# Performance work log

Hardware: AMD Instinct MI355X
Metric: run time of the kernel (lower is better)

Reference implementation:

```python
import jax, jax.numpy as jnp
import numpy as np
from math import sqrt

D_MODEL = 1024
B, T = 4, 4096


def setup_inputs() -> dict:
    key = jax.random.key(0)
    kx, kqk, kvo = jax.random.split(key, 3)
    x = jax.random.normal(kx, (B, T, D_MODEL), dtype=jnp.float32)
    # xavier_uniform for square [D, D]: limit = sqrt(6 / (D + D))
    limit = sqrt(6.0 / (2 * D_MODEL))
    QK = jax.random.uniform(kqk, (D_MODEL, D_MODEL), minval=-limit, maxval=limit, dtype=jnp.float32)
    VO = jax.random.uniform(kvo, (D_MODEL, D_MODEL), minval=-limit, maxval=limit, dtype=jnp.float32)
    return {"x": x, "QK": QK, "VO": VO}


def reference(x, QK, VO):
    d_model = QK.shape[0]
    # scores[b,t,u] = x[b,t,:] @ QK @ x[b,u,:]  -- precompute xQK once
    xQK = jnp.einsum('btd,de->bte', x, QK)                 # [B,T,D]
    scores = jnp.einsum('bte,bue->btu', xQK, x) / sqrt(d_model)  # [B,T,T]
    attn = jax.nn.softmax(scores, axis=2)
    # out[b,t,e] = attn @ x @ VO
    av = jnp.einsum('btu,bud->btd', attn, x)               # [B,T,D]
    return jnp.einsum('btd,de->bte', av, VO)
```

## Files before the change

kernel.cpp:

```cpp
#include <hip/hip_runtime.h>
#include <hip/hip_bf16.h>


#define BB 4
#define TT 4096
#define DD 1024

typedef __attribute__((ext_vector_type(8))) short bf16x8;
typedef __attribute__((ext_vector_type(4))) float f32x4;

__device__ __forceinline__ void gll16(const void* g, void* l) {
  __builtin_amdgcn_global_load_lds(
      (__attribute__((address_space(1))) void*)g,
      (__attribute__((address_space(3))) void*)l, 16, 0, 0);
}

#define WAIT_VM(n) asm volatile("s_waitcnt vmcnt(" #n ")" ::: "memory")
#define CFENCE     asm volatile("" ::: "memory")
#define BARRIER    do { CFENCE; __builtin_amdgcn_s_barrier(); CFENCE; } while (0)

__global__ __launch_bounds__(256) void xprep_k(const float* __restrict__ in,
                                               __hip_bfloat16* __restrict__ rm,
                                               __hip_bfloat16* __restrict__ cm,
                                               int R, int C, long bs) {
  in += (long)blockIdx.z * bs; rm += (long)blockIdx.z * bs; cm += (long)blockIdx.z * bs;
  __shared__ __hip_bfloat16 tile[64][65];
  int c0 = blockIdx.x * 64, r0 = blockIdx.y * 64;
  int tx = threadIdx.x & 63, ty = threadIdx.x >> 6;
#pragma unroll
  for (int i = 0; i < 16; ++i) {
    int r = ty + i * 4;
    __hip_bfloat16 v = __float2bfloat16(in[(long)(r0 + r) * C + c0 + tx]);
    tile[r][tx] = v;
    rm[(long)(r0 + r) * C + c0 + tx] = v;
  }
  __syncthreads();
#pragma unroll
  for (int i = 0; i < 16; ++i) {
    int c = ty + i * 4;
    cm[(long)(c0 + c) * R + r0 + tx] = tile[tx][c];
  }
}

__global__ __launch_bounds__(256) void transpose_cast_k(const float* __restrict__ in,
                                                        __hip_bfloat16* __restrict__ out,
                                                        int R, int C) {
  __shared__ __hip_bfloat16 tile[64][65];
  int c0 = blockIdx.x * 64, r0 = blockIdx.y * 64;
  int tx = threadIdx.x & 63, ty = threadIdx.x >> 6;
#pragma unroll
  for (int i = 0; i < 16; ++i) {
    int r = ty + i * 4;
    tile[r][tx] = __float2bfloat16(in[(long)(r0 + r) * C + c0 + tx]);
  }
  __syncthreads();
#pragma unroll
  for (int i = 0; i < 16; ++i) {
    int c = ty + i * 4;
    out[(long)(c0 + c) * R + r0 + tx] = tile[tx][c];
  }
}

__global__ __launch_bounds__(256) void zero_f32_k(float* __restrict__ p, int n) {
  int i = blockIdx.x * 256 + threadIdx.x;
  if (i < n) p[i] = 0.f;
}

template <typename OUT_T, int EPI>
__global__ __launch_bounds__(512, 2) void gemm256(
    const __hip_bfloat16* __restrict__ A,
    const __hip_bfloat16* __restrict__ Bt,
    OUT_T* __restrict__ C,
    int M, int N, int K, float alpha,
    long sAz, long sBz, long sCz, float* __restrict__ lsum,
    int cx, int cy) {
  __shared__ alignas(16) char smem[131072];
  A  += (long)blockIdx.z * sAz;
  Bt += (long)blockIdx.z * sBz;
  C  += (long)blockIdx.z * sCz;

  const int lin = blockIdx.x + gridDim.x * blockIdx.y;
  const int xcd = lin & 7;
  const int s   = lin >> 3;
  const int rpc = cx * cy;
  const int r   = xcd + 8 * (s / rpc);
  const int p   = s % rpc;
  const int rx  = gridDim.x / cx;
  const int bx  = (r % rx) * cx + p % cx;
  const int by  = (r / rx) * cy + p / cx;

  const int tid  = threadIdx.x;
  const int lane = tid & 63;
  const int wid  = tid >> 6;
  const int wr   = wid >> 2;
  const int wc   = wid & 3;
  const long m0 = (long)bx * 256;
  const long n0 = (long)by * 256;
  const int NT = K >> 6;

  const int srow = tid >> 3;
  const int sswz = (tid & 7) ^ (srow & 7);
  const __hip_bfloat16* gA = A  + (m0 + srow) * (long)K + sswz * 8;
  const __hip_bfloat16* gB = Bt + (n0 + srow) * (long)K + sswz * 8;

#define STG_A(s_, c_, D_) gll16(gA + (long)(c_) * 64 * K + (long)(s_) * 64, \
                                smem + (D_) + (c_) * 8192 + wid * 1024)
#define STG_B(s_, c_, D_) gll16(gB + (long)(c_) * 64 * K + (long)(s_) * 64, \
                                smem + (D_) + 32768 + (c_) * 8192 + wid * 1024)

  const int fr = lane & 15, l4 = lane >> 4, f7 = lane & 7;
  const char* a00 = smem +         (wr * 128 + fr) * 128 + ((l4    ) ^ f7) * 16;
  const char* a01 = smem +         (wr * 128 + fr) * 128 + ((4 | l4) ^ f7) * 16;
  const char* b00 = smem + 32768 + (wc * 64  + fr) * 128 + ((l4    ) ^ f7) * 16;
  const char* b01 = smem + 32768 + (wc * 64  + fr) * 128 + ((4 | l4) ^ f7) * 16;
  const char* a10 = a00 + 65536; const char* a11 = a01 + 65536;
  const char* b10 = b00 + 65536; const char* b11 = b01 + 65536;

  bf16x8 aq[4][2], bq[4][2];
#define RD_A(p0, p1, MIOFF)                                         \
  _Pragma("unroll") for (int mi_ = 0; mi_ < 4; ++mi_) {             \
    aq[mi_][0] = *(const bf16x8*)((p0) + ((MIOFF) + mi_) * 2048);   \
    aq[mi_][1] = *(const bf16x8*)((p1) + ((MIOFF) + mi_) * 2048);   \
  }
#define RD_B(p0, p1, NI0)                                           \
  _Pragma("unroll") for (int ni_ = 0; ni_ < 2; ++ni_) {             \
    bq[(NI0) + ni_][0] = *(const bf16x8*)((p0) + ((NI0) + ni_) * 2048); \
    bq[(NI0) + ni_][1] = *(const bf16x8*)((p1) + ((NI0) + ni_) * 2048); \
  }

  f32x4 acc[8][4];
#pragma unroll
  for (int mi = 0; mi < 8; ++mi)
#pragma unroll
    for (int ni = 0; ni < 4; ++ni)
      acc[mi][ni] = (f32x4){0.f, 0.f, 0.f, 0.f};

#define MFMA16(MI0, NI0)                                                       \
  do {                                                                         \
    __builtin_amdgcn_s_setprio(1);                                             \
    _Pragma("unroll") for (int ks_ = 0; ks_ < 2; ++ks_)                        \
    _Pragma("unroll") for (int mi_ = 0; mi_ < 4; ++mi_)                        \
    _Pragma("unroll") for (int ni_ = 0; ni_ < 2; ++ni_)                        \
      acc[(MI0) + mi_][(NI0) + ni_] = __builtin_amdgcn_mfma_f32_16x16x32_bf16( \
          aq[mi_][ks_], bq[(NI0) + ni_][ks_], acc[(MI0) + mi_][(NI0) + ni_],   \
          0, 0, 0);                                                            \
    __builtin_amdgcn_s_setprio(0);                                             \
  } while (0)

#pragma unroll
  for (int c = 0; c < 4; ++c) STG_A(0, c, 0);
#pragma unroll
  for (int c = 0; c < 4; ++c) STG_B(0, c, 0);
  STG_B(1, 0, 65536); STG_B(1, 1, 65536);
  WAIT_VM(2);
  BARRIER;

  for (int t2 = 0; t2 < NT; t2 += 2) {
    const bool g = (t2 + 2 < NT);
    RD_B(b00, b01, 0); RD_A(a00, a01, 0);
    STG_B(t2 + 1, 2, 65536); STG_B(t2 + 1, 3, 65536);
    STG_A(t2 + 1, 0, 65536); STG_A(t2 + 1, 1, 65536);
    BARRIER; MFMA16(0, 0);
    RD_B(b00, b01, 2);
    STG_A(t2 + 1, 2, 65536); STG_A(t2 + 1, 3, 65536);
    BARRIER; MFMA16(0, 2);
    RD_A(a00, a01, 4);
    BARRIER; MFMA16(4, 2);
    if (g) { STG_B(t2 + 2, 0, 0); STG_B(t2 + 2, 1, 0); WAIT_VM(2); }
    else   { WAIT_VM(0); }
    BARRIER; MFMA16(4, 0);
    RD_B(b10, b11, 0); RD_A(a10, a11, 0);
    if (g) { STG_B(t2 + 2, 2, 0); STG_B(t2 + 2, 3, 0);
             STG_A(t2 + 2, 0, 0); STG_A(t2 + 2, 1, 0); }
    BARRIER; MFMA16(0, 0);
    RD_B(b10, b11, 2);
    if (g) { STG_A(t2 + 2, 2, 0); STG_A(t2 + 2, 3, 0); }
    BARRIER; MFMA16(0, 2);
    RD_A(a10, a11, 4);
    BARRIER; MFMA16(4, 2);
    if (g) { STG_B(t2 + 3, 0, 65536); STG_B(t2 + 3, 1, 65536); WAIT_VM(2); }
    BARRIER; MFMA16(4, 0);
  }

  if constexpr (EPI == 2) {
    float* lred = (float*)smem;
    __syncthreads();
    for (int i = tid; i < 1024; i += 512) lred[i] = 0.f;
    __syncthreads();
#pragma unroll
    for (int mi = 0; mi < 8; ++mi) {
#pragma unroll
      for (int r_ = 0; r_ < 4; ++r_) {
        const int rloc = wr * 128 + mi * 16 + (l4 << 2) + r_;
        const long row = m0 + rloc;
        float rs = 0.f;
#pragma unroll
        for (int ni = 0; ni < 4; ++ni) {
          float e = __expf(acc[mi][ni][r_] * alpha);
          long col = n0 + wc * 64 + ni * 16 + fr;
          C[row * (long)N + col] = (OUT_T)__float2bfloat16(e);
          rs += e;
        }
        rs += __shfl_xor(rs, 1); rs += __shfl_xor(rs, 2);
        rs += __shfl_xor(rs, 4); rs += __shfl_xor(rs, 8);
        if (fr == 0) lred[rloc * 4 + wc] = rs;
      }
    }
    __syncthreads();
    if (tid < 256) {
      float s4 = lred[tid * 4] + lred[tid * 4 + 1] + lred[tid * 4 + 2] + lred[tid * 4 + 3];
      atomicAdd(&lsum[(long)blockIdx.z * M + m0 + tid], s4);
    }
  } else if constexpr (EPI == 3) {
#pragma unroll
    for (int mi = 0; mi < 8; ++mi) {
      const long row = m0 + wr * 128 + mi * 16 + (l4 << 2);
      float4 lv = *(const float4*)&lsum[(long)blockIdx.z * M + row];
      float inv[4] = {1.f / lv.x, 1.f / lv.y, 1.f / lv.z, 1.f / lv.w};
#pragma unroll
      for (int ni = 0; ni < 4; ++ni) {
        long col = n0 + wc * 64 + ni * 16 + fr;
#pragma unroll
        for (int r_ = 0; r_ < 4; ++r_)
          C[(row + r_) * (long)N + col] = (OUT_T)__float2bfloat16(acc[mi][ni][r_] * inv[r_]);
      }
    }
  } else {
#pragma unroll
    for (int mi = 0; mi < 8; ++mi)
#pragma unroll
      for (int ni = 0; ni < 4; ++ni)
#pragma unroll
        for (int r_ = 0; r_ < 4; ++r_) {
          long row = m0 + wr * 128 + mi * 16 + (l4 << 2) + r_;
          long col = n0 + wc * 64 + ni * 16 + fr;
          float v = acc[mi][ni][r_] * alpha;
          if constexpr (EPI == 0)
            C[row * (long)N + col] = v;
          else
            C[row * (long)N + col] = (OUT_T)__float2bfloat16(v);
        }
  }
#undef STG_A
#undef STG_B
#undef RD_A
#undef RD_B
#undef MFMA16
}

extern "C" void kernel_launch(void* const* d_in, const int* in_sizes, int n_in,
                              void* d_out, int out_size, void* d_ws, size_t ws_size,
                              hipStream_t stream) {
  const float* x  = (const float*)d_in[0];
  const float* QK = (const float*)d_in[1];
  const float* VO = (const float*)d_in[2];
  char* ws = (char*)d_ws;

  const long MB = 1l << 20;
  __hip_bfloat16* QKT  = (__hip_bfloat16*)(ws);
  float*          lsum = (float*)(ws);
  __hip_bfloat16* VOT  = (__hip_bfloat16*)(ws + 2 * MB);
  __hip_bfloat16* xb   = (__hip_bfloat16*)(ws + 4 * MB);
  __hip_bfloat16* xT   = (__hip_bfloat16*)(ws + 36 * MB);
  __hip_bfloat16* attn = (__hip_bfloat16*)(ws + 68 * MB);
  __hip_bfloat16* xqk  = (__hip_bfloat16*)d_out;

  const long NTOK = (long)BB * TT;
  const long bstride = (long)TT * DD;
  const long aslot = (long)TT * TT;

  xprep_k<<<dim3(DD / 64, TT / 64, BB), 256, 0, stream>>>(x, xb, xT, TT, DD, bstride);
  transpose_cast_k<<<dim3(16, 16, 1), 256, 0, stream>>>(QK, QKT, DD, DD);
  transpose_cast_k<<<dim3(16, 16, 1), 256, 0, stream>>>(VO, VOT, DD, DD);

  gemm256<__hip_bfloat16, 1><<<dim3(TT / 256, DD / 256, BB), 512, 0, stream>>>(
      xb, QKT, xqk, TT, DD, DD, 1.0f, bstride, 0, bstride, nullptr, 2, 4);

  zero_f32_k<<<(int)(NTOK / 256), 256, 0, stream>>>(lsum, (int)NTOK);

  gemm256<__hip_bfloat16, 2><<<dim3(TT / 256, TT / 256, BB), 512, 0, stream>>>(
      xqk, xb, attn, TT, TT, DD, 0.03125f, bstride, bstride, aslot, lsum, 4, 8);

  gemm256<__hip_bfloat16, 3><<<dim3(TT / 256, DD / 256, BB), 512, 0, stream>>>(
      attn, xT, xb, TT, DD, TT, 1.0f, aslot, bstride, bstride, lsum, 2, 4);

  gemm256<float, 0><<<dim3((int)(NTOK / 256), DD / 256, 1), 512, 0, stream>>>(
      xb, VOT, (float*)d_out, (int)NTOK, DD, DD, 1.0f, 0, 0, 0, nullptr, 8, 4);
}
```

Measured before the change: 340.8 us.

## Make scores GEMM persistent over four N-tiles with prefetch and staged epilogue

The scores GEMM now launches 256 blocks, and each one computes four consecutive 256-column tiles in turn instead of one. The first K-steps of the next tile are prefetched into LDS while the current tile's exp/sum epilogue runs. That epilogue now stages bf16 results through padded shared memory so global stores are coalesced 16-byte writes, and it accumulates row sums in LDS across tiles, needing one atomic per row per block. This aims to hide epilogue and prologue latency and cut scattered 2-byte stores and atomics. In exchange it uses more shared memory, adds extra per-row barriers in the epilogue, and launches fewer blocks, which may underfill the GPU.

```diff
diff --git a/kernel.cpp b/kernel.cpp
--- a/kernel.cpp
+++ b/kernel.cpp
@@ -66,7 +66,7 @@
   if (i < n) p[i] = 0.f;
 }
 
-template <typename OUT_T, int EPI>
+template <typename OUT_T, int EPI, int TILES>
 __global__ __launch_bounds__(512, 2) void gemm256(
     const __hip_bfloat16* __restrict__ A,
     const __hip_bfloat16* __restrict__ Bt,
@@ -74,20 +74,32 @@
     int M, int N, int K, float alpha,
     long sAz, long sBz, long sCz, float* __restrict__ lsum,
     int cx, int cy) {
-  __shared__ alignas(16) char smem[131072];
-  A  += (long)blockIdx.z * sAz;
-  Bt += (long)blockIdx.z * sBz;
-  C  += (long)blockIdx.z * sCz;
-
-  const int lin = blockIdx.x + gridDim.x * blockIdx.y;
-  const int xcd = lin & 7;
-  const int s   = lin >> 3;
-  const int rpc = cx * cy;
-  const int r   = xcd + 8 * (s / rpc);
-  const int p   = s % rpc;
-  const int rx  = gridDim.x / cx;
-  const int bx  = (r % rx) * cx + p % cx;
-  const int by  = (r / rx) * cy + p / cx;
+  __shared__ alignas(16) char smem[(EPI == 2) ? 152064 : 131072];
+
+  constexpr bool MULTI = (TILES > 1);
+  int zi, bx;
+  long n0;
+  int q = 0;
+  if constexpr (MULTI) {
+    zi = blockIdx.x >> 6;
+    bx = (blockIdx.x >> 2) & 15;
+    q  = blockIdx.x & 3;
+    n0 = (long)(q * 4) * 256;
+  } else {
+    zi = blockIdx.z;
+    const int lin = blockIdx.x + gridDim.x * blockIdx.y;
+    const int xcd = lin & 7;
+    const int s   = lin >> 3;
+    const int rpc = cx * cy;
+    const int r   = xcd + 8 * (s / rpc);
+    const int p   = s % rpc;
+    const int rx  = gridDim.x / cx;
+    bx = (r % rx) * cx + p % cx;
+    n0 = (long)((r / rx) * cy + p / cx) * 256;
+  }
+  const __hip_bfloat16* Az  = A  + (long)zi * sAz;
+  const __hip_bfloat16* Btz = Bt + (long)zi * sBz;
+  C += (long)zi * sCz;
 
   const int tid  = threadIdx.x;
   const int lane = tid & 63;
@@ -95,18 +107,23 @@
   const int wr   = wid >> 2;
   const int wc   = wid & 3;
   const long m0 = (long)bx * 256;
-  const long n0 = (long)by * 256;
   const int NT = K >> 6;
 
   const int srow = tid >> 3;
   const int sswz = (tid & 7) ^ (srow & 7);
-  const __hip_bfloat16* gA = A  + (m0 + srow) * (long)K + sswz * 8;
-  const __hip_bfloat16* gB = Bt + (n0 + srow) * (long)K + sswz * 8;
+  const __hip_bfloat16* gA = Az + (m0 + srow) * (long)K + sswz * 8;
+  const __hip_bfloat16* gB = Btz + (n0 + srow) * (long)K + sswz * 8;
 
 #define STG_A(s_, c_, D_) gll16(gA + (long)(c_) * 64 * K + (long)(s_) * 64, \
                                 smem + (D_) + (c_) * 8192 + wid * 1024)
 #define STG_B(s_, c_, D_) gll16(gB + (long)(c_) * 64 * K + (long)(s_) * 64, \
                                 smem + (D_) + 32768 + (c_) * 8192 + wid * 1024)
+#define STAGE16() do { \
+    STG_A(0, 0, 0); STG_A(0, 1, 0); STG_A(0, 2, 0); STG_A(0, 3, 0);          \
+    STG_B(0, 0, 0); STG_B(0, 1, 0); STG_B(0, 2, 0); STG_B(0, 3, 0);          \
+    STG_B(1, 0, 65536); STG_B(1, 1, 65536); STG_B(1, 2, 65536); STG_B(1, 3, 65536); \
+    STG_A(1, 0, 65536); STG_A(1, 1, 65536); STG_A(1, 2, 65536); STG_A(1, 3, 65536); \
+  } while (0)
 
   const int fr = lane & 15, l4 = lane >> 4, f7 = lane & 7;
   const char* a00 = smem +         (wr * 128 + fr) * 128 + ((l4    ) ^ f7) * 16;
@@ -129,11 +146,6 @@
   }
 
   f32x4 acc[8][4];
-#pragma unroll
-  for (int mi = 0; mi < 8; ++mi)
-#pragma unroll
-    for (int ni = 0; ni < 4; ++ni)
-      acc[mi][ni] = (f32x4){0.f, 0.f, 0.f, 0.f};
 
 #define MFMA16(MI0, NI0)                                                       \
   do {                                                                         \
@@ -147,102 +159,136 @@
     __builtin_amdgcn_s_setprio(0);                                             \
   } while (0)
 
-#pragma unroll
-  for (int c = 0; c < 4; ++c) STG_A(0, c, 0);
-#pragma unroll
-  for (int c = 0; c < 4; ++c) STG_B(0, c, 0);
-  STG_B(1, 0, 65536); STG_B(1, 1, 65536);
-  WAIT_VM(2);
+  float* lred = (float*)(smem + 131072);
+  char*  pch  = smem + 135168;
+
+  STAGE16();
+  WAIT_VM(8);
+  if constexpr (EPI == 2) {
+    for (int i = tid; i < 1024; i += 512) lred[i] = 0.f;
+  }
   BARRIER;
 
-  for (int t2 = 0; t2 < NT; t2 += 2) {
-    const bool g = (t2 + 2 < NT);
-    RD_B(b00, b01, 0); RD_A(a00, a01, 0);
-    STG_B(t2 + 1, 2, 65536); STG_B(t2 + 1, 3, 65536);
-    STG_A(t2 + 1, 0, 65536); STG_A(t2 + 1, 1, 65536);
-    BARRIER; MFMA16(0, 0);
-    RD_B(b00, b01, 2);
-    STG_A(t2 + 1, 2, 65536); STG_A(t2 + 1, 3, 65536);
-    BARRIER; MFMA16(0, 2);
-    RD_A(a00, a01, 4);
-    BARRIER; MFMA16(4, 2);
-    if (g) { STG_B(t2 + 2, 0, 0); STG_B(t2 + 2, 1, 0); WAIT_VM(2); }
-    else   { WAIT_VM(0); }
-    BARRIER; MFMA16(4, 0);
-    RD_B(b10, b11, 0); RD_A(a10, a11, 0);
-    if (g) { STG_B(t2 + 2, 2, 0); STG_B(t2 + 2, 3, 0);
-             STG_A(t2 + 2, 0, 0); STG_A(t2 + 2, 1, 0); }
-    BARRIER; MFMA16(0, 0);
-    RD_B(b10, b11, 2);
-    if (g) { STG_A(t2 + 2, 2, 0); STG_A(t2 + 2, 3, 0); }
-    BARRIER; MFMA16(0, 2);
-    RD_A(a10, a11, 4);
-    BARRIER; MFMA16(4, 2);
-    if (g) { STG_B(t2 + 3, 0, 65536); STG_B(t2 + 3, 1, 65536); WAIT_VM(2); }
-    BARRIER; MFMA16(4, 0);
+#pragma unroll 1
+  for (int tau = 0; tau < TILES; ++tau) {
+    const bool seam = MULTI && (tau > 0);
+#pragma unroll
+    for (int mi = 0; mi < 8; ++mi)
+#pragma unroll
+      for (int ni = 0; ni < 4; ++ni)
+        acc[mi][ni] = (f32x4){0.f, 0.f, 0.f, 0.f};
+
+    for (int t2 = 0; t2 < NT; t2 += 2) {
+      const bool g = (t2 + 2 < NT);
+      RD_B(b00, b01, 0); RD_A(a00, a01, 0);
+      if (t2) { STG_B(t2 + 1, 2, 65536); STG_B(t2 + 1, 3, 65536);
+                STG_A(t2 + 1, 0, 65536); STG_A(t2 + 1, 1, 65536); }
+      BARRIER; MFMA16(0, 0);
+      RD_B(b00, b01, 2);
+      if (t2) { STG_A(t2 + 1, 2, 65536); STG_A(t2 + 1, 3, 65536); }
+      BARRIER; MFMA16(0, 2);
+      RD_A(a00, a01, 4);
+      BARRIER; MFMA16(4, 2);
+      if (g) { STG_B(t2 + 2, 0, 0); STG_B(t2 + 2, 1, 0); }
+      if (t2 == 0) { if (seam) { WAIT_VM(18); } else { WAIT_VM(2); } }
+      else if (g)  { WAIT_VM(2); }
+      else         { WAIT_VM(0); }
+      BARRIER; MFMA16(4, 0);
+      RD_B(b10, b11, 0); RD_A(a10, a11, 0);
+      if (g) { STG_B(t2 + 2, 2, 0); STG_B(t2 + 2, 3, 0);
+               STG_A(t2 + 2, 0, 0); STG_A(t2 + 2, 1, 0); }
+      BARRIER; MFMA16(0, 0);
+      RD_B(b10, b11, 2);
+      if (g) { STG_A(t2 + 2, 2, 0); STG_A(t2 + 2, 3, 0); }
+      BARRIER; MFMA16(0, 2);
+      RD_A(a10, a11, 4);
+      BARRIER; MFMA16(4, 2);
+      if (g) { STG_B(t2 + 3, 0, 65536); STG_B(t2 + 3, 1, 65536); WAIT_VM(2); }
+      BARRIER; MFMA16(4, 0);
+    }
+    BARRIER;
+
+    const long n0c = n0;
+    if (MULTI && tau + 1 < TILES) {
+      n0 = (long)(q * 4 + tau + 1) * 256;
+      gB = Btz + (n0 + srow) * (long)K + sswz * 8;
+      STAGE16();
+      WAIT_VM(8);
+    }
+
+    if constexpr (EPI == 2) {
+#pragma unroll 1
+      for (int mi = 0; mi < 8; ++mi) {
+#pragma unroll
+        for (int r_ = 0; r_ < 4; ++r_) {
+          const int lr = wr * 16 + (l4 << 2) + r_;
+          float rs = 0.f;
+#pragma unroll
+          for (int ni = 0; ni < 4; ++ni) {
+            float e = __expf(acc[mi][ni][r_] * alpha);
+            *(__hip_bfloat16*)(pch + lr * 528 + (wc * 64 + ni * 16 + fr) * 2) =
+                __float2bfloat16(e);
+            rs += e;
+          }
+          rs += __shfl_xor(rs, 1); rs += __shfl_xor(rs, 2);
+          rs += __shfl_xor(rs, 4); rs += __shfl_xor(rs, 8);
+          if (fr == 0)
+            lred[(wr * 128 + mi * 16 + (l4 << 2) + r_) * 4 + wc] += rs;
+        }
+        __syncthreads();
+#pragma unroll
+        for (int it = 0; it < 2; ++it) {
+          int idx = it * 512 + tid;
+          int lr2 = idx >> 5, cs = idx & 31;
+          uint4 v = *(const uint4*)(pch + lr2 * 528 + cs * 16);
+          long grow = m0 + ((lr2 < 16) ? (mi * 16 + lr2)
+                                       : (128 + mi * 16 + lr2 - 16));
+          *(uint4*)&C[grow * (long)N + n0c + cs * 8] = v;
+        }
+        __syncthreads();
+      }
+    } else if constexpr (EPI == 3) {
+#pragma unroll
+      for (int mi = 0; mi < 8; ++mi) {
+        const long row = m0 + wr * 128 + mi * 16 + (l4 << 2);
+        float4 lv = *(const float4*)&lsum[(long)zi * M + row];
+        float inv[4] = {1.f / lv.x, 1.f / lv.y, 1.f / lv.z, 1.f / lv.w};
+#pragma unroll
+        for (int ni = 0; ni < 4; ++ni) {
+          long col = n0c + wc * 64 + ni * 16 + fr;
+#pragma unroll
+          for (int r_ = 0; r_ < 4; ++r_)
+            C[(row + r_) * (long)N + col] = (OUT_T)__float2bfloat16(acc[mi][ni][r_] * inv[r_]);
+        }
+      }
+    } else {
+#pragma unroll
+      for (int mi = 0; mi < 8; ++mi)
+#pragma unroll
+        for (int ni = 0; ni < 4; ++ni)
+#pragma unroll
+          for (int r_ = 0; r_ < 4; ++r_) {
+            long row = m0 + wr * 128 + mi * 16 + (l4 << 2) + r_;
+            long col = n0c + wc * 64 + ni * 16 + fr;
+            float v = acc[mi][ni][r_] * alpha;
+            if constexpr (EPI == 0)
+              C[row * (long)N + col] = v;
+            else
+              C[row * (long)N + col] = (OUT_T)__float2bfloat16(v);
+          }
+    }
   }
 
   if constexpr (EPI == 2) {
-    float* lred = (float*)smem;
-    __syncthreads();
-    for (int i = tid; i < 1024; i += 512) lred[i] = 0.f;
-    __syncthreads();
-#pragma unroll
-    for (int mi = 0; mi < 8; ++mi) {
-#pragma unroll
-      for (int r_ = 0; r_ < 4; ++r_) {
-        const int rloc = wr * 128 + mi * 16 + (l4 << 2) + r_;
-        const long row = m0 + rloc;
-        float rs = 0.f;
-#pragma unroll
-        for (int ni = 0; ni < 4; ++ni) {
-          float e = __expf(acc[mi][ni][r_] * alpha);
-          long col = n0 + wc * 64 + ni * 16 + fr;
-          C[row * (long)N + col] = (OUT_T)__float2bfloat16(e);
-          rs += e;
-        }
-        rs += __shfl_xor(rs, 1); rs += __shfl_xor(rs, 2);
-        rs += __shfl_xor(rs, 4); rs += __shfl_xor(rs, 8);
-        if (fr == 0) lred[rloc * 4 + wc] = rs;
-      }
-    }
     __syncthreads();
     if (tid < 256) {
       float s4 = lred[tid * 4] + lred[tid * 4 + 1] + lred[tid * 4 + 2] + lred[tid * 4 + 3];
-      atomicAdd(&lsum[(long)blockIdx.z * M + m0 + tid], s4);
+      atomicAdd(&lsum[(long)zi * M + m0 + tid], s4);
     }
-  } else if constexpr (EPI == 3) {
-#pragma unroll
-    for (int mi = 0; mi < 8; ++mi) {
-      const long row = m0 + wr * 128 + mi * 16 + (l4 << 2);
-      float4 lv = *(const float4*)&lsum[(long)blockIdx.z * M + row];
-      float inv[4] = {1.f / lv.x, 1.f / lv.y, 1.f / lv.z, 1.f / lv.w};
-#pragma unroll
-      for (int ni = 0; ni < 4; ++ni) {
-        long col = n0 + wc * 64 + ni * 16 + fr;
-#pragma unroll
-        for (int r_ = 0; r_ < 4; ++r_)
-          C[(row + r_) * (long)N + col] = (OUT_T)__float2bfloat16(acc[mi][ni][r_] * inv[r_]);
-      }
-    }
-  } else {
-#pragma unroll
-    for (int mi = 0; mi < 8; ++mi)
-#pragma unroll
-      for (int ni = 0; ni < 4; ++ni)
-#pragma unroll
-        for (int r_ = 0; r_ < 4; ++r_) {
-          long row = m0 + wr * 128 + mi * 16 + (l4 << 2) + r_;
-          long col = n0 + wc * 64 + ni * 16 + fr;
-          float v = acc[mi][ni][r_] * alpha;
-          if constexpr (EPI == 0)
-            C[row * (long)N + col] = v;
-          else
-            C[row * (long)N + col] = (OUT_T)__float2bfloat16(v);
-        }
   }
 #undef STG_A
 #undef STG_B
+#undef STAGE16
 #undef RD_A
 #undef RD_B
 #undef MFMA16
@@ -273,17 +319,17 @@
   transpose_cast_k<<<dim3(16, 16, 1), 256, 0, stream>>>(QK, QKT, DD, DD);
   transpose_cast_k<<<dim3(16, 16, 1), 256, 0, stream>>>(VO, VOT, DD, DD);
 
-  gemm256<__hip_bfloat16, 1><<<dim3(TT / 256, DD / 256, BB), 512, 0, stream>>>(
+  gemm256<__hip_bfloat16, 1, 1><<<dim3(TT / 256, DD / 256, BB), 512, 0, stream>>>(
       xb, QKT, xqk, TT, DD, DD, 1.0f, bstride, 0, bstride, nullptr, 2, 4);
 
   zero_f32_k<<<(int)(NTOK / 256), 256, 0, stream>>>(lsum, (int)NTOK);
 
-  gemm256<__hip_bfloat16, 2><<<dim3(TT / 256, TT / 256, BB), 512, 0, stream>>>(
-      xqk, xb, attn, TT, TT, DD, 0.03125f, bstride, bstride, aslot, lsum, 4, 8);
-
-  gemm256<__hip_bfloat16, 3><<<dim3(TT / 256, DD / 256, BB), 512, 0, stream>>>(
+  gemm256<__hip_bfloat16, 2, 4><<<dim3(256, 1, 1), 512, 0, stream>>>(
+      xqk, xb, attn, TT, TT, DD, 0.03125f, bstride, bstride, aslot, lsum, 0, 0);
+
+  gemm256<__hip_bfloat16, 3, 1><<<dim3(TT / 256, DD / 256, BB), 512, 0, stream>>>(
       attn, xT, xb, TT, DD, TT, 1.0f, aslot, bstride, bstride, lsum, 2, 4);
 
-  gemm256<float, 0><<<dim3((int)(NTOK / 256), DD / 256, 1), 512, 0, stream>>>(
+  gemm256<float, 0, 1><<<dim3((int)(NTOK / 256), DD / 256, 1), 512, 0, stream>>>(
       xb, VOT, (float*)d_out, (int)NTOK, DD, DD, 1.0f, 0, 0, 0, nullptr, 8, 4);
 }
```

New measurement: 544.8 us. +59.9%, slower.
